# Performance work log

Hardware: AMD Instinct MI355X
Metric: run time of the kernel (lower is better)

The kernel has to match this reference:

```python
import jax, jax.numpy as jnp
import numpy as np

# par: dt=0.05, tau_m=10.0 -> alpha = 1 - dt/tau_m; v_th = 2.0
ALPHA = 1.0 - 0.05 / 10.0
V_TH = 2.0


def setup_inputs() -> dict:
    key = jax.random.key(0)
    k1, k2 = jax.random.split(key)
    B, T, N = 128, 1000, 1024
    x = jax.random.normal(k1, (B, T, N), dtype=jnp.float32)
    # torch init: normal(mean=0, std=1/sqrt(N))
    w = jax.random.normal(k2, (N,), dtype=jnp.float32) * (1.0 / np.sqrt(N))
    return {"x": x, "w": w}


def reference(x, w):
    """Runs the NeuronClass.__call__ LIF step over all T timesteps.

    v_t = alpha * v_{t-1} + x_t @ w - v_th * stop_grad(z_{t-1})
    z_t = 1[v_t - v_th > 0]
    Returns (v_seq, z_seq), each [B, T].
    """
    B, T, N = x.shape
    # Precompute the input current for all timesteps (same math as per-step x_t @ w,
    # but a single large GEMM instead of T small GEMVs).
    drive = jnp.einsum('btn,n->bt', x, w)  # [B, T]

    def step(carry, i_t):
        v, z = carry
        v = ALPHA * v + i_t - V_TH * jax.lax.stop_gradient(z)
        z = (v - V_TH > 0).astype(v.dtype)
        return (v, z), (v, z)

    v0 = jnp.zeros((B,), dtype=x.dtype)
    z0 = jnp.zeros((B,), dtype=x.dtype)
    _, (v_seq, z_seq) = jax.lax.scan(step, (v0, z0), drive.T)  # scanned outputs [T, B]
    return v_seq.T, z_seq.T
```

## Files before the change

### kernel.cpp

```cpp
#include <hip/hip_runtime.h>


#define ALPHA 0.995f
#define V_TH 2.0f

constexpr int B = 128;
constexpr int T = 1000;
constexpr int N = 1024;

typedef float f32x4 __attribute__((ext_vector_type(4)));

__global__ __launch_bounds__(256) void lif_dot_kernel(
    const float* __restrict__ x, const float* __restrict__ w,
    float* __restrict__ drive_t) {
    const int lane = threadIdx.x & 63;
    const int gwave = blockIdx.x * 4 + (threadIdx.x >> 6);
    const int base_row = gwave * 4;

    const float* wp = w + lane * 4;
    const f32x4 w0 = *(const f32x4*)(wp);
    const f32x4 w1 = *(const f32x4*)(wp + 256);
    const f32x4 w2 = *(const f32x4*)(wp + 512);
    const f32x4 w3 = *(const f32x4*)(wp + 768);

#pragma unroll
    for (int i = 0; i < 4; i += 2) {
        const f32x4* xr0 = (const f32x4*)(x + (long long)(base_row + i) * N + lane * 4);
        const f32x4* xr1 = (const f32x4*)((const float*)xr0 + N);
        const f32x4 a0 = __builtin_nontemporal_load(xr0);
        const f32x4 a1 = __builtin_nontemporal_load(xr0 + 64);
        const f32x4 a2 = __builtin_nontemporal_load(xr0 + 128);
        const f32x4 a3 = __builtin_nontemporal_load(xr0 + 192);
        const f32x4 b0 = __builtin_nontemporal_load(xr1);
        const f32x4 b1 = __builtin_nontemporal_load(xr1 + 64);
        const f32x4 b2 = __builtin_nontemporal_load(xr1 + 128);
        const f32x4 b3 = __builtin_nontemporal_load(xr1 + 192);

        double s0 = (double)a0.x*w0.x + (double)a0.y*w0.y + (double)a0.z*w0.z + (double)a0.w*w0.w;
        double s1 = (double)a1.x*w1.x + (double)a1.y*w1.y + (double)a1.z*w1.z + (double)a1.w*w1.w;
        double s2 = (double)a2.x*w2.x + (double)a2.y*w2.y + (double)a2.z*w2.z + (double)a2.w*w2.w;
        double s3 = (double)a3.x*w3.x + (double)a3.y*w3.y + (double)a3.z*w3.z + (double)a3.w*w3.w;
        double t0 = (double)b0.x*w0.x + (double)b0.y*w0.y + (double)b0.z*w0.z + (double)b0.w*w0.w;
        double t1 = (double)b1.x*w1.x + (double)b1.y*w1.y + (double)b1.z*w1.z + (double)b1.w*w1.w;
        double t2 = (double)b2.x*w2.x + (double)b2.y*w2.y + (double)b2.z*w2.z + (double)b2.w*w2.w;
        double t3 = (double)b3.x*w3.x + (double)b3.y*w3.y + (double)b3.z*w3.z + (double)b3.w*w3.w;
        double accA = (s0 + s1) + (s2 + s3);
        double accB = (t0 + t1) + (t2 + t3);

#pragma unroll
        for (int off = 32; off >= 1; off >>= 1) {
            accA += __shfl_down(accA, off);
            accB += __shfl_down(accB, off);
        }

        if (lane == 0) {
            const int row = base_row + i;
            const int b1_ = row / T;
            const int t1_ = row - b1_ * T;
            drive_t[t1_ * B + b1_] = (float)accA;
            const int row2 = row + 1;
            const int b2_ = row2 / T;
            const int t2_ = row2 - b2_ * T;
            drive_t[t2_ * B + b2_] = (float)accB;
        }
    }
}

__global__ __launch_bounds__(512) void lif_scan_kernel(
    const float* __restrict__ drive_t, float* __restrict__ out) {
    __shared__ float s_drive[64 * B];
    __shared__ float s_v[B][65];
    __shared__ float s_z[B][65];
    const int tid = threadIdx.x;

    float v = 0.0f, z = 0.0f;
    for (int t0 = 0; t0 < T; t0 += 64) {
        const int TT = (T - t0 < 64) ? (T - t0) : 64;
        const int nq = (TT * B) / 4;

        const f32x4* src = (const f32x4*)(drive_t + t0 * B);
        f32x4* dst = (f32x4*)s_drive;
        for (int idx = tid; idx < nq; idx += 512)
            dst[idx] = src[idx];
        __syncthreads();

        if (tid < B) {
            float vv = v, zz = z;
            for (int j = 0; j < TT; ++j) {
                const float d = s_drive[j * B + tid];
                vv = ALPHA * vv + d - V_TH * zz;
                zz = (vv - V_TH > 0.0f) ? 1.0f : 0.0f;
                s_v[tid][j] = vv;
                s_z[tid][j] = zz;
            }
            v = vv; z = zz;
        }
        __syncthreads();

        const int qpb = TT / 4;
        for (int idx = tid; idx < nq; idx += 512) {
            const int bb = idx / qpb;
            const int j4 = (idx - bb * qpb) * 4;
            f32x4 vq = { s_v[bb][j4], s_v[bb][j4+1], s_v[bb][j4+2], s_v[bb][j4+3] };
            *(f32x4*)(out + (long long)bb * T + t0 + j4) = vq;
            f32x4 zq = { s_z[bb][j4], s_z[bb][j4+1], s_z[bb][j4+2], s_z[bb][j4+3] };
            *(f32x4*)(out + (long long)(B + bb) * T + t0 + j4) = zq;
        }
        __syncthreads();
    }
}

extern "C" void kernel_launch(void* const* d_in, const int* in_sizes, int n_in,
                              void* d_out, int out_size, void* d_ws, size_t ws_size,
                              hipStream_t stream) {
    const float* x = (const float*)d_in[0];
    const float* w = (const float*)d_in[1];
    float* out = (float*)d_out;
    float* drive_t = (float*)d_ws;

    lif_dot_kernel<<<8000, 256, 0, stream>>>(x, w, drive_t);
    lif_scan_kernel<<<1, 512, 0, stream>>>(drive_t, out);
}
```

Baseline: 686.6 us.

## Fuse dot and scan kernels with tile counters to overlap the scan

Merges the drive GEMV and the sequential LIF scan into one launch. Block 0 acts as a consumer that spins on per-tile atomic counters and scans each 8-timestep tile as soon as producer blocks finish it. Producer blocks are remapped so each covers a contiguous tile of timesteps across the batch, and each signals completion with an atomic add. This hides the serial scan behind the bandwidth-bound dot product, at the cost of a memset, spin-waiting, and reliance on block 0 being scheduled and on relaxed atomics giving correct visibility.

```diff
diff --git a/kernel.cpp b/kernel.cpp
--- a/kernel.cpp
+++ b/kernel.cpp
@@ -7,15 +7,74 @@
 constexpr int B = 128;
 constexpr int T = 1000;
 constexpr int N = 1024;
+constexpr int TILE_T = 8;
+constexpr int NTILES = T / TILE_T;
+constexpr int ROWS_PER_TILE = TILE_T * B;
 
 typedef float f32x4 __attribute__((ext_vector_type(4)));
 
-__global__ __launch_bounds__(256) void lif_dot_kernel(
+__global__ __launch_bounds__(256) void lif_fused_kernel(
     const float* __restrict__ x, const float* __restrict__ w,
-    float* __restrict__ drive_t) {
-    const int lane = threadIdx.x & 63;
-    const int gwave = blockIdx.x * 4 + (threadIdx.x >> 6);
-    const int base_row = gwave * 4;
+    float* __restrict__ out, float* __restrict__ drive_t,
+    unsigned int* __restrict__ tile_cnt) {
+    __shared__ float s_v[B][TILE_T + 1];
+    __shared__ float s_z[B][TILE_T + 1];
+    const int tid = threadIdx.x;
+
+    if (blockIdx.x == 0) {
+        float v = 0.0f, z = 0.0f;
+        for (int g = 0; g < NTILES; ++g) {
+            if (tid == 0) {
+                while (__hip_atomic_load(&tile_cnt[g], __ATOMIC_RELAXED,
+                                         __HIP_MEMORY_SCOPE_AGENT) <
+                       (unsigned)ROWS_PER_TILE)
+                    __builtin_amdgcn_s_sleep(8);
+            }
+            __syncthreads();
+
+            const int t0 = g * TILE_T;
+            if (tid < B) {
+                float d[TILE_T];
+#pragma unroll
+                for (int j = 0; j < TILE_T; ++j)
+                    d[j] = __hip_atomic_load(&drive_t[(t0 + j) * B + tid],
+                                             __ATOMIC_RELAXED,
+                                             __HIP_MEMORY_SCOPE_AGENT);
+                float vv = v, zz = z;
+#pragma unroll
+                for (int j = 0; j < TILE_T; ++j) {
+                    vv = ALPHA * vv + d[j] - V_TH * zz;
+                    zz = (vv - V_TH > 0.0f) ? 1.0f : 0.0f;
+                    s_v[tid][j] = vv;
+                    s_z[tid][j] = zz;
+                }
+                v = vv; z = zz;
+            }
+            __syncthreads();
+
+            {
+                const int bb = tid >> 1;
+                const int j4 = (tid & 1) * 4;
+                f32x4 vq = { s_v[bb][j4], s_v[bb][j4 + 1],
+                             s_v[bb][j4 + 2], s_v[bb][j4 + 3] };
+                *(f32x4*)(out + (long long)bb * T + t0 + j4) = vq;
+                f32x4 zq = { s_z[bb][j4], s_z[bb][j4 + 1],
+                             s_z[bb][j4 + 2], s_z[bb][j4 + 3] };
+                *(f32x4*)(out + (long long)(B + bb) * T + t0 + j4) = zq;
+            }
+            __syncthreads();
+        }
+        return;
+    }
+
+    const int lane = tid & 63;
+    const int gwave = (blockIdx.x - 1) * 4 + (tid >> 6);
+    const int base = gwave * 4;
+    const int g  = base >> 10;
+    const int rem = base & 1023;
+    const int b  = rem >> 3;
+    const int j0 = rem & 7;
+    const int t0 = g * TILE_T + j0;
 
     const float* wp = w + lane * 4;
     const f32x4 w0 = *(const f32x4*)(wp);
@@ -23,9 +82,11 @@
     const f32x4 w2 = *(const f32x4*)(wp + 512);
     const f32x4 w3 = *(const f32x4*)(wp + 768);
 
+    const float* xb = x + ((long long)b * T + t0) * N + lane * 4;
+
 #pragma unroll
     for (int i = 0; i < 4; i += 2) {
-        const f32x4* xr0 = (const f32x4*)(x + (long long)(base_row + i) * N + lane * 4);
+        const f32x4* xr0 = (const f32x4*)(xb + (long long)i * N);
         const f32x4* xr1 = (const f32x4*)((const float*)xr0 + N);
         const f32x4 a0 = __builtin_nontemporal_load(xr0);
         const f32x4 a1 = __builtin_nontemporal_load(xr0 + 64);
@@ -40,12 +101,12 @@
         double s1 = (double)a1.x*w1.x + (double)a1.y*w1.y + (double)a1.z*w1.z + (double)a1.w*w1.w;
         double s2 = (double)a2.x*w2.x + (double)a2.y*w2.y + (double)a2.z*w2.z + (double)a2.w*w2.w;
         double s3 = (double)a3.x*w3.x + (double)a3.y*w3.y + (double)a3.z*w3.z + (double)a3.w*w3.w;
-        double t0 = (double)b0.x*w0.x + (double)b0.y*w0.y + (double)b0.z*w0.z + (double)b0.w*w0.w;
-        double t1 = (double)b1.x*w1.x + (double)b1.y*w1.y + (double)b1.z*w1.z + (double)b1.w*w1.w;
-        double t2 = (double)b2.x*w2.x + (double)b2.y*w2.y + (double)b2.z*w2.z + (double)b2.w*w2.w;
-        double t3 = (double)b3.x*w3.x + (double)b3.y*w3.y + (double)b3.z*w3.z + (double)b3.w*w3.w;
+        double t0_ = (double)b0.x*w0.x + (double)b0.y*w0.y + (double)b0.z*w0.z + (double)b0.w*w0.w;
+        double t1_ = (double)b1.x*w1.x + (double)b1.y*w1.y + (double)b1.z*w1.z + (double)b1.w*w1.w;
+        double t2_ = (double)b2.x*w2.x + (double)b2.y*w2.y + (double)b2.z*w2.z + (double)b2.w*w2.w;
+        double t3_ = (double)b3.x*w3.x + (double)b3.y*w3.y + (double)b3.z*w3.z + (double)b3.w*w3.w;
         double accA = (s0 + s1) + (s2 + s3);
-        double accB = (t0 + t1) + (t2 + t3);
+        double accB = (t0_ + t1_) + (t2_ + t3_);
 
 #pragma unroll
         for (int off = 32; off >= 1; off >>= 1) {
@@ -54,60 +115,17 @@
         }
 
         if (lane == 0) {
-            const int row = base_row + i;
-            const int b1_ = row / T;
-            const int t1_ = row - b1_ * T;
-            drive_t[t1_ * B + b1_] = (float)accA;
-            const int row2 = row + 1;
-            const int b2_ = row2 / T;
-            const int t2_ = row2 - b2_ * T;
-            drive_t[t2_ * B + b2_] = (float)accB;
+            __hip_atomic_store(&drive_t[(t0 + i) * B + b], (float)accA,
+                               __ATOMIC_RELAXED, __HIP_MEMORY_SCOPE_AGENT);
+            __hip_atomic_store(&drive_t[(t0 + i + 1) * B + b], (float)accB,
+                               __ATOMIC_RELAXED, __HIP_MEMORY_SCOPE_AGENT);
         }
     }
-}
 
-__global__ __launch_bounds__(512) void lif_scan_kernel(
-    const float* __restrict__ drive_t, float* __restrict__ out) {
-    __shared__ float s_drive[64 * B];
-    __shared__ float s_v[B][65];
-    __shared__ float s_z[B][65];
-    const int tid = threadIdx.x;
-
-    float v = 0.0f, z = 0.0f;
-    for (int t0 = 0; t0 < T; t0 += 64) {
-        const int TT = (T - t0 < 64) ? (T - t0) : 64;
-        const int nq = (TT * B) / 4;
-
-        const f32x4* src = (const f32x4*)(drive_t + t0 * B);
-        f32x4* dst = (f32x4*)s_drive;
-        for (int idx = tid; idx < nq; idx += 512)
-            dst[idx] = src[idx];
-        __syncthreads();
-
-        if (tid < B) {
-            float vv = v, zz = z;
-            for (int j = 0; j < TT; ++j) {
-                const float d = s_drive[j * B + tid];
-                vv = ALPHA * vv + d - V_TH * zz;
-                zz = (vv - V_TH > 0.0f) ? 1.0f : 0.0f;
-                s_v[tid][j] = vv;
-                s_z[tid][j] = zz;
-            }
-            v = vv; z = zz;
-        }
-        __syncthreads();
-
-        const int qpb = TT / 4;
-        for (int idx = tid; idx < nq; idx += 512) {
-            const int bb = idx / qpb;
-            const int j4 = (idx - bb * qpb) * 4;
-            f32x4 vq = { s_v[bb][j4], s_v[bb][j4+1], s_v[bb][j4+2], s_v[bb][j4+3] };
-            *(f32x4*)(out + (long long)bb * T + t0 + j4) = vq;
-            f32x4 zq = { s_z[bb][j4], s_z[bb][j4+1], s_z[bb][j4+2], s_z[bb][j4+3] };
-            *(f32x4*)(out + (long long)(B + bb) * T + t0 + j4) = zq;
-        }
-        __syncthreads();
-    }
+    __syncthreads();
+    if (tid == 0)
+        __hip_atomic_fetch_add(&tile_cnt[g], 16u, __ATOMIC_RELAXED,
+                               __HIP_MEMORY_SCOPE_AGENT);
 }
 
 extern "C" void kernel_launch(void* const* d_in, const int* in_sizes, int n_in,
@@ -117,7 +135,10 @@
     const float* w = (const float*)d_in[1];
     float* out = (float*)d_out;
     float* drive_t = (float*)d_ws;
+    unsigned int* tile_cnt =
+        (unsigned int*)((char*)d_ws + 512 * 1024);
 
-    lif_dot_kernel<<<8000, 256, 0, stream>>>(x, w, drive_t);
-    lif_scan_kernel<<<1, 512, 0, stream>>>(drive_t, out);
+    hipMemsetAsync(tile_cnt, 0, NTILES * sizeof(unsigned int), stream);
+
+    lif_fused_kernel<<<8001, 256, 0, stream>>>(x, w, out, drive_t, tile_cnt);
 }
```

Result: slower. 717.3 us (+4.5%).

## Replace LDS-staged scan with per-thread register tiles and direct vector stores

Applied to the files above, without the earlier changes.

The single-block scan kernel drops its shared-memory staging of drive values and outputs. Each of 128 threads now loads a 40-step tile of its own drive column into registers, runs the recurrence, and writes v and z straight to global memory as float4 stores. This removes three __syncthreads per tile and the LDS transpose, but the per-thread stores are strided by T across lanes, so they coalesce poorly, and the loads are scalar. The scan is a small part of the total time next to the 512MB dot-product pass.

```diff
diff --git a/kernel.cpp b/kernel.cpp
--- a/kernel.cpp
+++ b/kernel.cpp
@@ -7,6 +7,7 @@
 constexpr int B = 128;
 constexpr int T = 1000;
 constexpr int N = 1024;
+constexpr int TILE_T = 40;
 
 typedef float f32x4 __attribute__((ext_vector_type(4)));
 
@@ -66,47 +67,31 @@
     }
 }
 
-__global__ __launch_bounds__(512) void lif_scan_kernel(
+__global__ __launch_bounds__(128) void lif_scan_kernel(
     const float* __restrict__ drive_t, float* __restrict__ out) {
-    __shared__ float s_drive[64 * B];
-    __shared__ float s_v[B][65];
-    __shared__ float s_z[B][65];
-    const int tid = threadIdx.x;
+    const int b = threadIdx.x;
+    float v = 0.0f, z = 0.0f;
+    for (int t0 = 0; t0 < T; t0 += TILE_T) {
+        float d[TILE_T];
+#pragma unroll
+        for (int j = 0; j < TILE_T; ++j)
+            d[j] = drive_t[(t0 + j) * B + b];
 
-    float v = 0.0f, z = 0.0f;
-    for (int t0 = 0; t0 < T; t0 += 64) {
-        const int TT = (T - t0 < 64) ? (T - t0) : 64;
-        const int nq = (TT * B) / 4;
-
-        const f32x4* src = (const f32x4*)(drive_t + t0 * B);
-        f32x4* dst = (f32x4*)s_drive;
-        for (int idx = tid; idx < nq; idx += 512)
-            dst[idx] = src[idx];
-        __syncthreads();
-
-        if (tid < B) {
-            float vv = v, zz = z;
-            for (int j = 0; j < TT; ++j) {
-                const float d = s_drive[j * B + tid];
-                vv = ALPHA * vv + d - V_TH * zz;
-                zz = (vv - V_TH > 0.0f) ? 1.0f : 0.0f;
-                s_v[tid][j] = vv;
-                s_z[tid][j] = zz;
+        float* vout = out + (long long)b * T + t0;
+        float* zout = out + (long long)(B + b) * T + t0;
+#pragma unroll
+        for (int j4 = 0; j4 < TILE_T; j4 += 4) {
+            f32x4 vq, zq;
+#pragma unroll
+            for (int k = 0; k < 4; ++k) {
+                v = ALPHA * v + d[j4 + k] - V_TH * z;
+                z = (v - V_TH > 0.0f) ? 1.0f : 0.0f;
+                vq[k] = v;
+                zq[k] = z;
             }
-            v = vv; z = zz;
+            *(f32x4*)(vout + j4) = vq;
+            *(f32x4*)(zout + j4) = zq;
         }
-        __syncthreads();
-
-        const int qpb = TT / 4;
-        for (int idx = tid; idx < nq; idx += 512) {
-            const int bb = idx / qpb;
-            const int j4 = (idx - bb * qpb) * 4;
-            f32x4 vq = { s_v[bb][j4], s_v[bb][j4+1], s_v[bb][j4+2], s_v[bb][j4+3] };
-            *(f32x4*)(out + (long long)bb * T + t0 + j4) = vq;
-            f32x4 zq = { s_z[bb][j4], s_z[bb][j4+1], s_z[bb][j4+2], s_z[bb][j4+3] };
-            *(f32x4*)(out + (long long)(B + bb) * T + t0 + j4) = zq;
-        }
-        __syncthreads();
     }
 }
 
@@ -119,5 +104,5 @@
     float* drive_t = (float*)d_ws;
 
     lif_dot_kernel<<<8000, 256, 0, stream>>>(x, w, drive_t);
-    lif_scan_kernel<<<1, 512, 0, stream>>>(drive_t, out);
+    lif_scan_kernel<<<1, 128, 0, stream>>>(drive_t, out);
 }
```

Result: faster. 669.8 us, median of 2 (-2.4%).
